# Kernel tuning notes

Hardware: AMD Instinct MI355X
Metric: run time of the kernel (lower is better)

## Reference

```python
import jax, jax.numpy as jnp
import numpy as np

B, N, D, E, HEADS = 2, 256, 768, 8192, 8
HD = D // HEADS
EPS = 1e-5


def _lin(x, w, b):
    return x @ w.T + b


def setup_inputs() -> dict:
    key = jax.random.key(0)
    ks = iter(jax.random.split(key, 64))

    def W(*s):
        return jax.random.normal(next(ks), s, jnp.float32) * 0.02

    inp = {
        "node_embeddings": jax.random.normal(next(ks), (B, N, D), jnp.float32),
        "edge_weights": jax.random.uniform(next(ks), (E,), jnp.float32),
        "edge_indices": jax.random.randint(next(ks), (E, 2), 0, N, jnp.int32),
        # object classifier: D->D->D//2->8
        "oc_w1": W(D, D), "oc_b1": jnp.zeros((D,), jnp.float32),
        "oc_w2": W(D // 2, D), "oc_b2": jnp.zeros((D // 2,), jnp.float32),
        "oc_w3": W(8, D // 2), "oc_b3": jnp.zeros((8,), jnp.float32),
        # importance predictor: D->D//2->D//4->1
        "ip_w1": W(D // 2, D), "ip_b1": jnp.zeros((D // 2,), jnp.float32),
        "ip_w2": W(D // 4, D // 2), "ip_b2": jnp.zeros((D // 4,), jnp.float32),
        "ip_w3": W(1, D // 4), "ip_b3": jnp.zeros((1,), jnp.float32),
        # relation classifier: 2D->D->D//2->8
        "rc_w1": W(D, 2 * D), "rc_b1": jnp.zeros((D,), jnp.float32),
        "rc_w2": W(D // 2, D), "rc_b2": jnp.zeros((D // 2,), jnp.float32),
        "rc_w3": W(8, D // 2), "rc_b3": jnp.zeros((8,), jnp.float32),
        # attention in/out projections
        "attn_in_w": W(3 * D, D), "attn_in_b": jnp.zeros((3 * D,), jnp.float32),
        "attn_out_w": W(D, D), "attn_out_b": jnp.zeros((D,), jnp.float32),
    }
    for l in range(3):
        inp[f"gnn{l}_ws"] = W(D, D)
        inp[f"gnn{l}_bs"] = jnp.zeros((D,), jnp.float32)
        inp[f"gnn{l}_wn"] = W(D, D)
        inp[f"gnn{l}_bn"] = jnp.zeros((D,), jnp.float32)
        inp[f"gnn{l}_g"] = jnp.ones((D,), jnp.float32)
        inp[f"gnn{l}_beta"] = jnp.zeros((D,), jnp.float32)
    return inp


def reference(node_embeddings, edge_weights, edge_indices,
              oc_w1, oc_b1, oc_w2, oc_b2, oc_w3, oc_b3,
              ip_w1, ip_b1, ip_w2, ip_b2, ip_w3, ip_b3,
              rc_w1, rc_b1, rc_w2, rc_b2, rc_w3, rc_b3,
              attn_in_w, attn_in_b, attn_out_w, attn_out_b,
              gnn0_ws, gnn0_bs, gnn0_wn, gnn0_bn, gnn0_g, gnn0_beta,
              gnn1_ws, gnn1_bs, gnn1_wn, gnn1_bn, gnn1_g, gnn1_beta,
              gnn2_ws, gnn2_bs, gnn2_wn, gnn2_bn, gnn2_g, gnn2_beta):
    x = node_embeddings  # [B,N,D]
    src, tgt = edge_indices[:, 0], edge_indices[:, 1]

    # object classifier (dropout is identity in eval)
    h = jax.nn.relu(_lin(x, oc_w1, oc_b1))
    h = jax.nn.relu(_lin(h, oc_w2, oc_b2))
    object_cls = jax.nn.softmax(_lin(h, oc_w3, oc_b3), axis=-1)

    # importance predictor
    h = jax.nn.relu(_lin(x, ip_w1, ip_b1))
    h = jax.nn.relu(_lin(h, ip_w2, ip_b2))
    importance = jax.nn.sigmoid(_lin(h, ip_w3, ip_b3))

    # 3 GNN layers: self-linear + weighted scatter-add neighbor aggregation
    g = x
    layers = [(gnn0_ws, gnn0_bs, gnn0_wn, gnn0_bn, gnn0_g, gnn0_beta),
              (gnn1_ws, gnn1_bs, gnn1_wn, gnn1_bn, gnn1_g, gnn1_beta),
              (gnn2_ws, gnn2_bs, gnn2_wn, gnn2_bn, gnn2_g, gnn2_beta)]
    for ws, bs, wn, bn, gm, bt in layers:
        self_f = _lin(g, ws, bs)
        # vectorized scatter-add: agg[b,tgt] += w_e * g[b,src]
        agg = jnp.zeros_like(g).at[:, tgt, :].add(edge_weights[None, :, None] * g[:, src, :])
        neigh_f = _lin(agg, wn, bn)
        o = jax.nn.relu(self_f + neigh_f)
        mu = o.mean(axis=-1, keepdims=True)
        var = o.var(axis=-1, keepdims=True)  # biased, as torch LayerNorm
        g = gm * (o - mu) / jnp.sqrt(var + EPS) + bt

    # multi-head self-attention (torch MultiheadAttention, batch_first)
    qkv = _lin(g, attn_in_w, attn_in_b)  # [B,N,3D]
    q, k, v = jnp.split(qkv, 3, axis=-1)

    def heads(t):
        return t.reshape(B, N, HEADS, HD).transpose(0, 2, 1, 3)  # [B,H,N,hd]

    q, k, v = heads(q), heads(k), heads(v)
    scores = jnp.einsum('bhqd,bhkd->bhqk', q, k) / jnp.sqrt(jnp.float32(HD))
    attn = jax.nn.softmax(scores, axis=-1)
    ctx = jnp.einsum('bhqk,bhkd->bhqd', attn, v).transpose(0, 2, 1, 3).reshape(B, N, D)
    attended = _lin(ctx, attn_out_w, attn_out_b)  # [B,N,D]
    attn_weights = attn.mean(axis=1)  # torch averages heads -> [B,N,N]

    # all O(N^2) upper-triangular pairs, same (i<j) row-major order as the loop
    ii, jj = np.triu_indices(N, k=1)
    pair = jnp.concatenate([attended[:, ii, :], attended[:, jj, :]], axis=-1)  # [B,P,2D]
    h = jax.nn.relu(_lin(pair, rc_w1, rc_b1))
    h = jax.nn.relu(_lin(h, rc_w2, rc_b2))
    relation = jax.nn.softmax(_lin(h, rc_w3, rc_b3), axis=-1)  # [B,P,8]

    return (object_cls, relation, importance, attended, attn_weights)
```

## Files before the change

kernel.cpp:

```cpp
#include <hip/hip_runtime.h>
#include <hip/hip_bf16.h>

typedef __bf16 bf16;
typedef __bf16 bf16x4 __attribute__((ext_vector_type(4)));
typedef __bf16 bf16x8 __attribute__((ext_vector_type(8)));
typedef float  f32x4  __attribute__((ext_vector_type(4)));

#define NB 2
#define NN 256
#define DD 768
#define EE 8192
#define NPAIR 32640

__device__ inline float wred_sum(float v) {
#pragma unroll
  for (int o = 32; o > 0; o >>= 1) v += __shfl_down(v, o, 64);
  return v;
}
__device__ inline float wred_max(float v) {
#pragma unroll
  for (int o = 32; o > 0; o >>= 1) v = fmaxf(v, __shfl_down(v, o, 64));
  return v;
}

typedef const __attribute__((address_space(1))) void GASV;
typedef __attribute__((address_space(3))) void LASV;
__device__ __forceinline__ void async_cp16(const void* g, void* l) {
  __builtin_amdgcn_global_load_lds((GASV*)g, (LASV*)l, 16, 0, 0);
}

struct CJob { const float* s; bf16* d; int n; };
struct CJobs { CJob j[15]; };
__global__ __launch_bounds__(256) void convert_jobs(CJobs jobs) {
  const CJob jb = jobs.j[blockIdx.y];
  int nv = jb.n >> 2;
  for (int i = blockIdx.x * 256 + threadIdx.x; i < nv; i += gridDim.x * 256) {
    float4 v = ((const float4*)jb.s)[i];
    bf16x4 pk = { (bf16)v.x, (bf16)v.y, (bf16)v.z, (bf16)v.w };
    *(bf16x4*)(jb.d + 4 * i) = pk;
  }
}

__global__ __launch_bounds__(128) void linear_mfma(
    const bf16* __restrict__ X, const bf16* __restrict__ W, int ldw, int wofs,
    const float* __restrict__ bias, const float* __restrict__ addF,
    bf16* __restrict__ outB, float* __restrict__ outF,
    int N, int K, int act)
{
  int tid = threadIdx.x;
  int wave = tid >> 6, lane = tid & 63, lr = lane & 15, lq = lane >> 4;
  int m0 = (blockIdx.x * 2 + wave) * 16;
  int n0 = blockIdx.y * 32;
  const bf16* xrow = X + (size_t)(m0 + lr) * K;
  const bf16* wbase = W + (size_t)wofs;
  f32x4 acc[2] = {};
  for (int k = 0; k < K; k += 32) {
    bf16x8 a = *(const bf16x8*)(xrow + k + lq * 8);
    bf16x8 b0 = *(const bf16x8*)(wbase + (size_t)(n0 + lr) * ldw + k + lq * 8);
    bf16x8 b1 = *(const bf16x8*)(wbase + (size_t)(n0 + 16 + lr) * ldw + k + lq * 8);
    acc[0] = __builtin_amdgcn_mfma_f32_16x16x32_bf16(a, b0, acc[0], 0, 0, 0);
    acc[1] = __builtin_amdgcn_mfma_f32_16x16x32_bf16(a, b1, acc[1], 0, 0, 0);
  }
#pragma unroll
  for (int t = 0; t < 2; ++t) {
    int col = n0 + t * 16 + lr;
    float bv = bias ? bias[col] : 0.0f;
#pragma unroll
    for (int r = 0; r < 4; ++r) {
      int row = m0 + lq * 4 + r;
      size_t o = (size_t)row * N + col;
      float v = acc[t][r] + bv;
      if (addF) v += addF[o];
      if (act) v = fmaxf(v, 0.0f);
      if (outB) outB[o] = (bf16)v;
      if (outF) outF[o] = v;
    }
  }
}

__global__ __launch_bounds__(256) void build_buckets(
    const int* __restrict__ eidx, int* __restrict__ estart, int* __restrict__ bucket)
{
  __shared__ int tg[EE];
  __shared__ int cnt[256];
  __shared__ int sst[257];
  int t = threadIdx.x;
  cnt[t] = 0;
  for (int e = t; e < EE; e += 256) tg[e] = eidx[2 * e + 1];
  __syncthreads();
  for (int e = t; e < EE; e += 256) atomicAdd(&cnt[tg[e]], 1);
  __syncthreads();
  if (t == 0) { int s = 0; for (int i = 0; i < 256; ++i) { sst[i] = s; s += cnt[i]; } sst[256] = s; }
  __syncthreads();
  estart[t] = sst[t];
  if (t == 0) estart[256] = sst[256];
  cnt[t] = sst[t];
  __syncthreads();
  for (int e = t; e < EE; e += 256) {
    int p = atomicAdd(&cnt[tg[e]], 1);
    bucket[p] = e;
  }
}

__global__ __launch_bounds__(256) void gnn_agg(
    const bf16* __restrict__ g, const float* __restrict__ ew, const int* __restrict__ eidx,
    const int* __restrict__ estart, const int* __restrict__ bucket, bf16* __restrict__ agg)
{
  __shared__ int   ssrc[256];
  __shared__ float sw[256];
  int tgt = blockIdx.x, b = blockIdx.y, t = threadIdx.x;
  int s = estart[tgt], e = estart[tgt + 1];
  s = max(0, min(s, EE));
  e = max(s, min(e, EE));
  const bf16* gb = g + (size_t)b * NN * DD;
  float a0 = 0, a1 = 0, a2 = 0, a3 = 0;
  for (int base = s; base < e; base += 256) {
    int nchunk = min(256, e - base);
    if (t < nchunk) {
      int eid = bucket[base + t];
      eid = max(0, min(eid, EE - 1));
      ssrc[t] = eidx[2 * eid] & (NN - 1);
      sw[t] = ew[eid];
    }
    __syncthreads();
    if (t < 192) {
      for (int q = 0; q < nchunk; ++q) {
        float w = sw[q];
        bf16x4 v = *(const bf16x4*)(gb + (size_t)ssrc[q] * DD + 4 * t);
        a0 += w * (float)v[0]; a1 += w * (float)v[1];
        a2 += w * (float)v[2]; a3 += w * (float)v[3];
      }
    }
    __syncthreads();
  }
  if (t < 192) {
    bf16x4 o = { (bf16)a0, (bf16)a1, (bf16)a2, (bf16)a3 };
    *(bf16x4*)(agg + ((size_t)b * NN + tgt) * DD + 4 * t) = o;
  }
}

__global__ __launch_bounds__(256) void layer_norm(
    const float* __restrict__ o, const float* __restrict__ gm,
    const float* __restrict__ bt, bf16* __restrict__ gout)
{
  __shared__ float red[8];
  int row = blockIdx.x, t = threadIdx.x;
  const float* orow = o + (size_t)row * DD;
  float v0 = orow[t], v1 = orow[t + 256], v2 = orow[t + 512];
  float s = v0 + v1 + v2;
  float q = v0 * v0 + v1 * v1 + v2 * v2;
  float ws_ = wred_sum(s), wq = wred_sum(q);
  if ((t & 63) == 0) { red[t >> 6] = ws_; red[4 + (t >> 6)] = wq; }
  __syncthreads();
  float S = red[0] + red[1] + red[2] + red[3];
  float Q = red[4] + red[5] + red[6] + red[7];
  float mu = S * (1.0f / 768.0f);
  float var = Q * (1.0f / 768.0f) - mu * mu;
  float rstd = rsqrtf(var + 1e-5f);
  bf16* gr = gout + (size_t)row * DD;
  gr[t]       = (bf16)(gm[t]       * (v0 - mu) * rstd + bt[t]);
  gr[t + 256] = (bf16)(gm[t + 256] * (v1 - mu) * rstd + bt[t + 256]);
  gr[t + 512] = (bf16)(gm[t + 512] * (v2 - mu) * rstd + bt[t + 512]);
}

__global__ __launch_bounds__(256) void attn_kernel(
    const bf16* __restrict__ qkv, float* __restrict__ probs, bf16* __restrict__ ctx)
{
  __shared__ float qs[96];
  __shared__ float ps[256];
  __shared__ float part[192];
  __shared__ float red[8];
  int qi = blockIdx.x, h = blockIdx.y, b = blockIdx.z, t = threadIdx.x;
  const bf16* qrow = qkv + ((size_t)(b * NN + qi)) * 2304 + h * 96;
  if (t < 96) qs[t] = (float)qrow[t];
  __syncthreads();
  const bf16* krow = qkv + ((size_t)(b * NN + t)) * 2304 + 768 + h * 96;
  float s = 0;
#pragma unroll
  for (int i = 0; i < 12; ++i) {
    bf16x8 kv = *(const bf16x8*)(krow + 8 * i);
#pragma unroll
    for (int j = 0; j < 8; ++j) s += qs[8 * i + j] * (float)kv[j];
  }
  s *= 0.10206207261596577f;
  float wm = wred_max(s);
  if ((t & 63) == 0) red[t >> 6] = wm;
  __syncthreads();
  float MX = fmaxf(fmaxf(red[0], red[1]), fmaxf(red[2], red[3]));
  float e = expf(s - MX);
  float wsum = wred_sum(e);
  if ((t & 63) == 0) red[4 + (t >> 6)] = wsum;
  __syncthreads();
  float SUM = red[4] + red[5] + red[6] + red[7];
  float p = e / SUM;
  ps[t] = p;
  probs[(((size_t)(b * 8 + h) * NN + qi) * NN) + t] = p;
  __syncthreads();
  if (t < 192) {
    int d = t % 96, half = t / 96;
    const bf16* vbase = qkv + (size_t)b * NN * 2304 + 1536 + h * 96 + d;
    float a0 = 0, a1 = 0, a2 = 0, a3 = 0;
    int k0 = half * 128;
    for (int k = k0; k < k0 + 128; k += 4) {
      a0 += ps[k]     * (float)vbase[(size_t)k * 2304];
      a1 += ps[k + 1] * (float)vbase[(size_t)(k + 1) * 2304];
      a2 += ps[k + 2] * (float)vbase[(size_t)(k + 2) * 2304];
      a3 += ps[k + 3] * (float)vbase[(size_t)(k + 3) * 2304];
    }
    part[t] = (a0 + a1) + (a2 + a3);
  }
  __syncthreads();
  if (t < 96)
    ctx[((size_t)(b * NN + qi)) * DD + h * 96 + t] = (bf16)(part[t] + part[t + 96]);
}

__global__ __launch_bounds__(256) void mean_heads(
    const float* __restrict__ probs, float* __restrict__ out)
{
  size_t idx = (size_t)blockIdx.x * 256 + threadIdx.x;
  int k = (int)(idx & 255);
  int qq = (int)((idx >> 8) & 255);
  int b = (int)(idx >> 16);
  float s = 0;
#pragma unroll
  for (int h = 0; h < 8; ++h) s += probs[(((size_t)(b * 8 + h) * NN + qq) * NN) + k];
  out[idx] = s * 0.125f;
}

__global__ __launch_bounds__(256) void fc8_softmax(
    const bf16* __restrict__ h, const float* __restrict__ w,
    const float* __restrict__ bias, float* __restrict__ out)
{
  __shared__ float sw3[8 * 384];
  int t = threadIdx.x;
  for (int i = t; i < 8 * 384; i += 256) sw3[i] = w[i];
  __syncthreads();
  int wave = t >> 6, lane = t & 63;
  int k0 = lane * 6;
#pragma unroll
  for (int i = 0; i < 4; ++i) {
    int r = blockIdx.x * 16 + wave * 4 + i;
    const bf16* hr = h + (size_t)r * 384;
    float hv[6];
#pragma unroll
    for (int j = 0; j < 6; ++j) hv[j] = (float)hr[k0 + j];
    float lg[8];
#pragma unroll
    for (int c = 0; c < 8; ++c) {
      float p = 0;
#pragma unroll
      for (int j = 0; j < 6; ++j) p += hv[j] * sw3[c * 384 + k0 + j];
      lg[c] = wred_sum(p);
    }
    if (lane == 0) {
      float mx = lg[0] + bias[0];
#pragma unroll
      for (int c = 0; c < 8; ++c) { lg[c] += bias[c]; mx = fmaxf(mx, lg[c]); }
      float ex[8], sum = 0;
#pragma unroll
      for (int c = 0; c < 8; ++c) { ex[c] = expf(lg[c] - mx); sum += ex[c]; }
      float inv = 1.0f / sum;
#pragma unroll
      for (int c = 0; c < 8; ++c) out[(size_t)r * 8 + c] = ex[c] * inv;
    }
  }
}

__global__ __launch_bounds__(256) void fc1_sigmoid(
    const bf16* __restrict__ h, const float* __restrict__ w,
    const float* __restrict__ bias, float* __restrict__ out)
{
  __shared__ float sw1[192];
  int t = threadIdx.x;
  if (t < 192) sw1[t] = w[t];
  __syncthreads();
  int wave = t >> 6, lane = t & 63;
  int k0 = lane * 3;
#pragma unroll
  for (int i = 0; i < 4; ++i) {
    int r = blockIdx.x * 16 + wave * 4 + i;
    const bf16* hr = h + (size_t)r * 192;
    float p = (float)hr[k0] * sw1[k0] + (float)hr[k0 + 1] * sw1[k0 + 1]
            + (float)hr[k0 + 2] * sw1[k0 + 2];
    float s = wred_sum(p);
    if (lane == 0) out[r] = 1.0f / (1.0f + expf(-(s + bias[0])));
  }
}

__global__ void make_pairs(int2* __restrict__ pairs)
{
  int i = blockIdx.x;
  int off = i * 255 - (i * (i - 1)) / 2;
  for (int j = i + 1 + threadIdx.x; j < NN; j += blockDim.x)
    pairs[off + (j - i - 1)] = make_int2(i, j);
}

__global__ __launch_bounds__(256) void h2_gemm(
    const bf16* __restrict__ Af, const bf16* __restrict__ Bf,
    const bf16* __restrict__ w2, const float* __restrict__ b2,
    const int2* __restrict__ pairs, bf16* __restrict__ h2)
{
  __shared__ bf16 sh1[128][32];
  __shared__ bf16 sw2[192][32];
  __shared__ int rA[128], rB[128];
  int tid = threadIdx.x;
  int r0 = blockIdx.x * 128;
  int bb = (r0 >= NPAIR) ? 1 : 0;
  int n0 = blockIdx.y * 192;
  if (tid < 128) {
    int2 ij = pairs[r0 - bb * NPAIR + tid];
    rA[tid] = (bb * NN + ij.x) * DD;
    rB[tid] = (bb * NN + ij.y) * DD;
  }
  __syncthreads();
  int row = tid >> 1, kh = (tid & 1) * 16;
  const bf16* ar = Af + rA[row] + kh;
  const bf16* br = Bf + rB[row] + kh;
  char* h1w = (char*)sh1 + row * 64 + (tid & 1) * 32;
  int wave = tid >> 6, lane = tid & 63, lr = lane & 15, lq = lane >> 4;
  int wr = wave >> 1, wc = wave & 1;
  f32x4 acc[4][6] = {};
  for (int k0 = 0; k0 < 768; k0 += 32) {
#pragma unroll
    for (int q = 0; q < 3; ++q)
      async_cp16(w2 + (size_t)(n0 + q * 64 + (tid >> 2)) * 768 + k0 + (tid & 3) * 8,
                 (char*)sw2 + q * 4096 + tid * 16);
    bf16x8 a0 = *(const bf16x8*)(ar + k0);
    bf16x8 a1 = *(const bf16x8*)(ar + k0 + 8);
    bf16x8 b0 = *(const bf16x8*)(br + k0);
    bf16x8 b1 = *(const bf16x8*)(br + k0 + 8);
    bf16x8 h0, h1v;
#pragma unroll
    for (int j = 0; j < 8; ++j) {
      h0[j]  = (bf16)fmaxf((float)a0[j] + (float)b0[j], 0.f);
      h1v[j] = (bf16)fmaxf((float)a1[j] + (float)b1[j], 0.f);
    }
    *(bf16x8*)h1w = h0;
    *(bf16x8*)(h1w + 16) = h1v;
    __syncthreads();
    bf16x8 af[4], bf_[6];
#pragma unroll
    for (int rf = 0; rf < 4; ++rf)
      af[rf] = *(const bf16x8*)((char*)sh1 + (wr * 64 + rf * 16 + lr) * 64 + lq * 16);
#pragma unroll
    for (int cf = 0; cf < 6; ++cf)
      bf_[cf] = *(const bf16x8*)((char*)sw2 + (wc * 96 + cf * 16 + lr) * 64 + lq * 16);
#pragma unroll
    for (int rf = 0; rf < 4; ++rf)
#pragma unroll
      for (int cf = 0; cf < 6; ++cf)
        acc[rf][cf] = __builtin_amdgcn_mfma_f32_16x16x32_bf16(af[rf], bf_[cf], acc[rf][cf], 0, 0, 0);
    __syncthreads();
  }
#pragma unroll
  for (int cf = 0; cf < 6; ++cf) {
    int col = n0 + wc * 96 + cf * 16 + lr;
    float bv = b2[col];
#pragma unroll
    for (int rf = 0; rf < 4; ++rf) {
#pragma unroll
      for (int r = 0; r < 4; ++r) {
        int prow = r0 + wr * 64 + rf * 16 + lq * 4 + r;
        h2[(size_t)prow * 384 + col] = (bf16)fmaxf(acc[rf][cf][r] + bv, 0.f);
      }
    }
  }
}

extern "C" void kernel_launch(void* const* d_in, const int* in_sizes, int n_in,
                              void* d_out, int out_size, void* d_ws, size_t ws_size,
                              hipStream_t stream)
{
  (void)in_sizes; (void)n_in; (void)out_size; (void)ws_size;
  const float* x    = (const float*)d_in[0];
  const float* ew   = (const float*)d_in[1];
  const int*   eidx = (const int*)d_in[2];
  const float* oc_w1 = (const float*)d_in[3];  const float* oc_b1 = (const float*)d_in[4];
  const float* oc_w2 = (const float*)d_in[5];  const float* oc_b2 = (const float*)d_in[6];
  const float* oc_w3 = (const float*)d_in[7];  const float* oc_b3 = (const float*)d_in[8];
  const float* ip_w1 = (const float*)d_in[9];  const float* ip_b1 = (const float*)d_in[10];
  const float* ip_w2 = (const float*)d_in[11]; const float* ip_b2 = (const float*)d_in[12];
  const float* ip_w3 = (const float*)d_in[13]; const float* ip_b3 = (const float*)d_in[14];
  const float* rc_w1 = (const float*)d_in[15]; const float* rc_b1 = (const float*)d_in[16];
  const float* rc_w2 = (const float*)d_in[17]; const float* rc_b2 = (const float*)d_in[18];
  const float* rc_w3 = (const float*)d_in[19]; const float* rc_b3 = (const float*)d_in[20];
  const float* at_iw = (const float*)d_in[21]; const float* at_ib = (const float*)d_in[22];
  const float* at_ow = (const float*)d_in[23]; const float* at_ob = (const float*)d_in[24];

  float* out = (float*)d_out;
  float* out_oc  = out;
  float* out_rel = out + 4096;
  float* out_imp = out + 526336;
  float* out_att = out + 526848;
  float* out_aw  = out + 920064;

  char* wp = (char*)d_ws;
  auto alloc = [&](size_t bytes) { char* p = wp; wp += (bytes + 255) & ~(size_t)255; return p; };
  bf16* h2B  = (bf16*)alloc((size_t)(2 * NPAIR) * 384 * 2);
  float* selfF = (float*)alloc((size_t)512 * 768 * 4);
  float* oBuf  = (float*)alloc((size_t)512 * 768 * 4);
  float* probs = (float*)alloc((size_t)2 * 8 * 256 * 256 * 4);
  bf16* AfB  = (bf16*)alloc((size_t)512 * 768 * 2);
  bf16* BfB  = (bf16*)alloc((size_t)512 * 768 * 2);
  bf16* xb   = (bf16*)alloc((size_t)512 * 768 * 2);
  bf16* g0   = (bf16*)alloc((size_t)512 * 768 * 2);
  bf16* g1   = (bf16*)alloc((size_t)512 * 768 * 2);
  bf16* hA   = (bf16*)alloc((size_t)512 * 768 * 2);
  bf16* hB   = (bf16*)alloc((size_t)512 * 384 * 2);
  bf16* hI1  = (bf16*)alloc((size_t)512 * 384 * 2);
  bf16* hI2  = (bf16*)alloc((size_t)512 * 192 * 2);
  bf16* aggB = (bf16*)alloc((size_t)512 * 768 * 2);
  bf16* qkv  = (bf16*)alloc((size_t)512 * 2304 * 2);
  bf16* ctx  = (bf16*)alloc((size_t)512 * 768 * 2);
  bf16* attB = (bf16*)alloc((size_t)512 * 768 * 2);
  bf16* w_oc1 = (bf16*)alloc((size_t)768 * 768 * 2);
  bf16* w_oc2 = (bf16*)alloc((size_t)384 * 768 * 2);
  bf16* w_ip1 = (bf16*)alloc((size_t)384 * 768 * 2);
  bf16* w_ip2 = (bf16*)alloc((size_t)192 * 384 * 2);
  bf16* w_rc1 = (bf16*)alloc((size_t)768 * 1536 * 2);
  bf16* w_rc2 = (bf16*)alloc((size_t)384 * 768 * 2);
  bf16* w_aiw = (bf16*)alloc((size_t)2304 * 768 * 2);
  bf16* w_aow = (bf16*)alloc((size_t)768 * 768 * 2);
  bf16* w_gnn[6];
  for (int i = 0; i < 6; ++i) w_gnn[i] = (bf16*)alloc((size_t)768 * 768 * 2);
  int2* pairs = (int2*)alloc((size_t)NPAIR * 8);
  int* estart = (int*)alloc(257 * 4);
  int* bucket = (int*)alloc((size_t)EE * 4);

  dim3 blk(256);
  dim3 blk128(128);

  CJobs cj;
  cj.j[0]  = { x,     xb,    512 * 768 };
  cj.j[1]  = { oc_w1, w_oc1, 768 * 768 };
  cj.j[2]  = { oc_w2, w_oc2, 384 * 768 };
  cj.j[3]  = { ip_w1, w_ip1, 384 * 768 };
  cj.j[4]  = { ip_w2, w_ip2, 192 * 384 };
  cj.j[5]  = { rc_w1, w_rc1, 768 * 1536 };
  cj.j[6]  = { rc_w2, w_rc2, 384 * 768 };
  cj.j[7]  = { at_iw, w_aiw, 2304 * 768 };
  cj.j[8]  = { at_ow, w_aow, 768 * 768 };
  for (int l = 0; l < 3; ++l) {
    cj.j[9 + 2 * l]  = { (const float*)d_in[25 + l * 6 + 0], w_gnn[2 * l],     768 * 768 };
    cj.j[10 + 2 * l] = { (const float*)d_in[25 + l * 6 + 2], w_gnn[2 * l + 1], 768 * 768 };
  }
  convert_jobs<<<dim3(128, 15), blk, 0, stream>>>(cj);

  build_buckets<<<1, blk, 0, stream>>>(eidx, estart, bucket);
  make_pairs<<<255, blk, 0, stream>>>(pairs);

  linear_mfma<<<dim3(16, 24), blk128, 0, stream>>>(xb, w_oc1, 768, 0, oc_b1, nullptr, hA, nullptr, 768, 768, 1);
  linear_mfma<<<dim3(16, 12), blk128, 0, stream>>>(hA, w_oc2, 768, 0, oc_b2, nullptr, hB, nullptr, 384, 768, 1);
  fc8_softmax<<<32, blk, 0, stream>>>(hB, oc_w3, oc_b3, out_oc);

  linear_mfma<<<dim3(16, 12), blk128, 0, stream>>>(xb, w_ip1, 768, 0, ip_b1, nullptr, hI1, nullptr, 384, 768, 1);
  linear_mfma<<<dim3(16, 6),  blk128, 0, stream>>>(hI1, w_ip2, 384, 0, ip_b2, nullptr, hI2, nullptr, 192, 384, 1);
  fc1_sigmoid<<<32, blk, 0, stream>>>(hI2, ip_w3, ip_b3, out_imp);

  const bf16* gcur = xb;
  bf16* gbufs[2] = { g0, g1 };
  for (int l = 0; l < 3; ++l) {
    const float* bs_ = (const float*)d_in[25 + l * 6 + 1];
    const float* bn_ = (const float*)d_in[25 + l * 6 + 3];
    const float* gm_ = (const float*)d_in[25 + l * 6 + 4];
    const float* bt_ = (const float*)d_in[25 + l * 6 + 5];
    linear_mfma<<<dim3(16, 24), blk128, 0, stream>>>(gcur, w_gnn[2 * l], 768, 0, bs_, nullptr, nullptr, selfF, 768, 768, 0);
    gnn_agg<<<dim3(256, 2), blk, 0, stream>>>(gcur, ew, eidx, estart, bucket, aggB);
    linear_mfma<<<dim3(16, 24), blk128, 0, stream>>>(aggB, w_gnn[2 * l + 1], 768, 0, bn_, selfF, nullptr, oBuf, 768, 768, 1);
    layer_norm<<<512, blk, 0, stream>>>(oBuf, gm_, bt_, gbufs[l & 1]);
    gcur = gbufs[l & 1];
  }

  linear_mfma<<<dim3(16, 72), blk128, 0, stream>>>(gcur, w_aiw, 768, 0, at_ib, nullptr, qkv, nullptr, 2304, 768, 0);
  attn_kernel<<<dim3(256, 8, 2), blk, 0, stream>>>(qkv, probs, ctx);
  mean_heads<<<512, blk, 0, stream>>>(probs, out_aw);
  linear_mfma<<<dim3(16, 24), blk128, 0, stream>>>(ctx, w_aow, 768, 0, at_ob, nullptr, attB, out_att, 768, 768, 0);

  linear_mfma<<<dim3(16, 24), blk128, 0, stream>>>(attB, w_rc1, 1536, 0,   rc_b1,  nullptr, AfB, nullptr, 768, 768, 0);
  linear_mfma<<<dim3(16, 24), blk128, 0, stream>>>(attB, w_rc1, 1536, 768, nullptr, nullptr, BfB, nullptr, 768, 768, 0);
  h2_gemm<<<dim3(510, 2), blk, 0, stream>>>(AfB, BfB, w_rc2, rc_b2, pairs, h2B);
  fc8_softmax<<<4080, blk, 0, stream>>>(h2B, rc_w3, rc_b3, out_rel);
}
```

Measured before the change: 549.8 us.

## Batch paired linears, fuse head-mean into attention, widen pair GEMM tile

Independent linear layers are now launched together through a two-job kernel that picks its job from blockIdx.z, cutting kernel launches. The per-head probability buffer and the mean_heads kernel are removed: attention atomically accumulates p/8 into the averaged output, which is zeroed with a memset first. The pair GEMM now computes all 384 output columns per 512-thread block, so the relu(A+B) hidden rows are built once instead of twice, and it uses a plane-split LDS layout. The trade-offs are atomic contention and a non-deterministic summation order for the attention weights, plus higher register and LDS pressure per block.

After: 562.3 us. 1.02x slower.

```diff
diff --git a/kernel.cpp b/kernel.cpp
--- a/kernel.cpp
+++ b/kernel.cpp
@@ -41,7 +41,7 @@
   }
 }
 
-__global__ __launch_bounds__(128) void linear_mfma(
+__device__ __forceinline__ void lin_body(
     const bf16* __restrict__ X, const bf16* __restrict__ W, int ldw, int wofs,
     const float* __restrict__ bias, const float* __restrict__ addF,
     bf16* __restrict__ outB, float* __restrict__ outF,
@@ -76,6 +76,27 @@
       if (outF) outF[o] = v;
     }
   }
+}
+
+__global__ __launch_bounds__(128) void linear_mfma(
+    const bf16* __restrict__ X, const bf16* __restrict__ W, int ldw, int wofs,
+    const float* __restrict__ bias, const float* __restrict__ addF,
+    bf16* __restrict__ outB, float* __restrict__ outF,
+    int N, int K, int act)
+{
+  lin_body(X, W, ldw, wofs, bias, addF, outB, outF, N, K, act);
+}
+
+struct LinJob {
+  const bf16* X; const bf16* W; int ldw; int wofs;
+  const float* bias; const float* addF; bf16* outB; float* outF;
+  int N, K, act, gy;
+};
+__global__ __launch_bounds__(128) void linear_mfma2(LinJob j0, LinJob j1)
+{
+  LinJob j = blockIdx.z ? j1 : j0;
+  if ((int)blockIdx.y >= j.gy) return;
+  lin_body(j.X, j.W, j.ldw, j.wofs, j.bias, j.addF, j.outB, j.outF, j.N, j.K, j.act);
 }
 
 __global__ __launch_bounds__(256) void build_buckets(
@@ -164,7 +185,7 @@
 }
 
 __global__ __launch_bounds__(256) void attn_kernel(
-    const bf16* __restrict__ qkv, float* __restrict__ probs, bf16* __restrict__ ctx)
+    const bf16* __restrict__ qkv, float* __restrict__ aw, bf16* __restrict__ ctx)
 {
   __shared__ float qs[96];
   __shared__ float ps[256];
@@ -194,7 +215,7 @@
   float SUM = red[4] + red[5] + red[6] + red[7];
   float p = e / SUM;
   ps[t] = p;
-  probs[(((size_t)(b * 8 + h) * NN + qi) * NN) + t] = p;
+  atomicAdd(&aw[((size_t)(b * NN + qi)) * NN + t], p * 0.125f);
   __syncthreads();
   if (t < 192) {
     int d = t % 96, half = t / 96;
@@ -214,19 +235,6 @@
     ctx[((size_t)(b * NN + qi)) * DD + h * 96 + t] = (bf16)(part[t] + part[t + 96]);
 }
 
-__global__ __launch_bounds__(256) void mean_heads(
-    const float* __restrict__ probs, float* __restrict__ out)
-{
-  size_t idx = (size_t)blockIdx.x * 256 + threadIdx.x;
-  int k = (int)(idx & 255);
-  int qq = (int)((idx >> 8) & 255);
-  int b = (int)(idx >> 16);
-  float s = 0;
-#pragma unroll
-  for (int h = 0; h < 8; ++h) s += probs[(((size_t)(b * 8 + h) * NN + qq) * NN) + k];
-  out[idx] = s * 0.125f;
-}
-
 __global__ __launch_bounds__(256) void fc8_softmax(
     const bf16* __restrict__ h, const float* __restrict__ w,
     const float* __restrict__ bias, float* __restrict__ out)
@@ -295,75 +303,71 @@
     pairs[off + (j - i - 1)] = make_int2(i, j);
 }
 
-__global__ __launch_bounds__(256) void h2_gemm(
+__global__ __launch_bounds__(512) void h2_gemm(
     const bf16* __restrict__ Af, const bf16* __restrict__ Bf,
     const bf16* __restrict__ w2, const float* __restrict__ b2,
     const int2* __restrict__ pairs, bf16* __restrict__ h2)
 {
-  __shared__ bf16 sh1[128][32];
-  __shared__ bf16 sw2[192][32];
+  __shared__ bf16 sh1[4][128][8];
+  __shared__ bf16 sw2[4][384][8];
   __shared__ int rA[128], rB[128];
   int tid = threadIdx.x;
   int r0 = blockIdx.x * 128;
   int bb = (r0 >= NPAIR) ? 1 : 0;
-  int n0 = blockIdx.y * 192;
   if (tid < 128) {
     int2 ij = pairs[r0 - bb * NPAIR + tid];
     rA[tid] = (bb * NN + ij.x) * DD;
     rB[tid] = (bb * NN + ij.y) * DD;
   }
   __syncthreads();
-  int row = tid >> 1, kh = (tid & 1) * 16;
-  const bf16* ar = Af + rA[row] + kh;
-  const bf16* br = Bf + rB[row] + kh;
-  char* h1w = (char*)sh1 + row * 64 + (tid & 1) * 32;
+  int hrow = tid >> 2, hch = tid & 3;
+  const bf16* ar = Af + rA[hrow] + hch * 8;
+  const bf16* br = Bf + rB[hrow] + hch * 8;
+  bf16* h1dst = &sh1[hch][hrow][0];
   int wave = tid >> 6, lane = tid & 63, lr = lane & 15, lq = lane >> 4;
-  int wr = wave >> 1, wc = wave & 1;
+  int wr = wave >> 2, wc = wave & 3;
   f32x4 acc[4][6] = {};
   for (int k0 = 0; k0 < 768; k0 += 32) {
 #pragma unroll
-    for (int q = 0; q < 3; ++q)
-      async_cp16(w2 + (size_t)(n0 + q * 64 + (tid >> 2)) * 768 + k0 + (tid & 3) * 8,
-                 (char*)sw2 + q * 4096 + tid * 16);
-    bf16x8 a0 = *(const bf16x8*)(ar + k0);
-    bf16x8 a1 = *(const bf16x8*)(ar + k0 + 8);
-    bf16x8 b0 = *(const bf16x8*)(br + k0);
-    bf16x8 b1 = *(const bf16x8*)(br + k0 + 8);
-    bf16x8 h0, h1v;
-#pragma unroll
-    for (int j = 0; j < 8; ++j) {
-      h0[j]  = (bf16)fmaxf((float)a0[j] + (float)b0[j], 0.f);
-      h1v[j] = (bf16)fmaxf((float)a1[j] + (float)b1[j], 0.f);
-    }
-    *(bf16x8*)h1w = h0;
-    *(bf16x8*)(h1w + 16) = h1v;
+    for (int q = 0; q < 3; ++q) {
+      int a = q * 512 + tid;
+      int plane = a / 384;
+      int rw = a - plane * 384;
+      async_cp16(w2 + (size_t)rw * 768 + k0 + plane * 8, (char*)sw2 + a * 16);
+    }
+    bf16x8 av = *(const bf16x8*)(ar + k0);
+    bf16x8 bv = *(const bf16x8*)(br + k0);
+    bf16x8 hv;
+#pragma unroll
+    for (int j = 0; j < 8; ++j)
+      hv[j] = (bf16)fmaxf((float)av[j] + (float)bv[j], 0.f);
+    *(bf16x8*)h1dst = hv;
     __syncthreads();
-    bf16x8 af[4], bf_[6];
+    bf16x8 af[4], bfr[6];
 #pragma unroll
     for (int rf = 0; rf < 4; ++rf)
-      af[rf] = *(const bf16x8*)((char*)sh1 + (wr * 64 + rf * 16 + lr) * 64 + lq * 16);
+      af[rf] = *(const bf16x8*)&sh1[lq][wr * 64 + rf * 16 + lr][0];
 #pragma unroll
     for (int cf = 0; cf < 6; ++cf)
-      bf_[cf] = *(const bf16x8*)((char*)sw2 + (wc * 96 + cf * 16 + lr) * 64 + lq * 16);
+      bfr[cf] = *(const bf16x8*)&sw2[lq][wc * 96 + cf * 16 + lr][0];
 #pragma unroll
     for (int rf = 0; rf < 4; ++rf)
 #pragma unroll
       for (int cf = 0; cf < 6; ++cf)
-        acc[rf][cf] = __builtin_amdgcn_mfma_f32_16x16x32_bf16(af[rf], bf_[cf], acc[rf][cf], 0, 0, 0);
+        acc[rf][cf] = __builtin_amdgcn_mfma_f32_16x16x32_bf16(af[rf], bfr[cf], acc[rf][cf], 0, 0, 0);
     __syncthreads();
   }
 #pragma unroll
   for (int cf = 0; cf < 6; ++cf) {
-    int col = n0 + wc * 96 + cf * 16 + lr;
-    float bv = b2[col];
-#pragma unroll
-    for (int rf = 0; rf < 4; ++rf) {
+    int col = wc * 96 + cf * 16 + lr;
+    float bv2 = b2[col];
+#pragma unroll
+    for (int rf = 0; rf < 4; ++rf)
 #pragma unroll
       for (int r = 0; r < 4; ++r) {
         int prow = r0 + wr * 64 + rf * 16 + lq * 4 + r;
-        h2[(size_t)prow * 384 + col] = (bf16)fmaxf(acc[rf][cf][r] + bv, 0.f);
+        h2[(size_t)prow * 384 + col] = (bf16)fmaxf(acc[rf][cf][r] + bv2, 0.f);
       }
-    }
   }
 }
 
@@ -399,7 +403,6 @@
   bf16* h2B  = (bf16*)alloc((size_t)(2 * NPAIR) * 384 * 2);
   float* selfF = (float*)alloc((size_t)512 * 768 * 4);
   float* oBuf  = (float*)alloc((size_t)512 * 768 * 4);
-  float* probs = (float*)alloc((size_t)2 * 8 * 256 * 256 * 4);
   bf16* AfB  = (bf16*)alloc((size_t)512 * 768 * 2);
   bf16* BfB  = (bf16*)alloc((size_t)512 * 768 * 2);
   bf16* xb   = (bf16*)alloc((size_t)512 * 768 * 2);
@@ -445,16 +448,22 @@
     cj.j[10 + 2 * l] = { (const float*)d_in[25 + l * 6 + 2], w_gnn[2 * l + 1], 768 * 768 };
   }
   convert_jobs<<<dim3(128, 15), blk, 0, stream>>>(cj);
+  hipMemsetAsync(out_aw, 0, (size_t)NB * NN * NN * 4, stream);
 
   build_buckets<<<1, blk, 0, stream>>>(eidx, estart, bucket);
   make_pairs<<<255, blk, 0, stream>>>(pairs);
 
-  linear_mfma<<<dim3(16, 24), blk128, 0, stream>>>(xb, w_oc1, 768, 0, oc_b1, nullptr, hA, nullptr, 768, 768, 1);
-  linear_mfma<<<dim3(16, 12), blk128, 0, stream>>>(hA, w_oc2, 768, 0, oc_b2, nullptr, hB, nullptr, 384, 768, 1);
+  {
+    LinJob a = { xb, w_oc1, 768, 0, oc_b1, nullptr, hA,  nullptr, 768, 768, 1, 24 };
+    LinJob b = { xb, w_ip1, 768, 0, ip_b1, nullptr, hI1, nullptr, 384, 768, 1, 12 };
+    linear_mfma2<<<dim3(16, 24, 2), blk128, 0, stream>>>(a, b);
+  }
+  {
+    LinJob a = { hA,  w_oc2, 768, 0, oc_b2, nullptr, hB,  nullptr, 384, 768, 1, 12 };
+    LinJob b = { hI1, w_ip2, 384, 0, ip_b2, nullptr, hI2, nullptr, 192, 384, 1, 6 };
+    linear_mfma2<<<dim3(16, 12, 2), blk128, 0, stream>>>(a, b);
+  }
   fc8_softmax<<<32, blk, 0, stream>>>(hB, oc_w3, oc_b3, out_oc);
-
-  linear_mfma<<<dim3(16, 12), blk128, 0, stream>>>(xb, w_ip1, 768, 0, ip_b1, nullptr, hI1, nullptr, 384, 768, 1);
-  linear_mfma<<<dim3(16, 6),  blk128, 0, stream>>>(hI1, w_ip2, 384, 0, ip_b2, nullptr, hI2, nullptr, 192, 384, 1);
   fc1_sigmoid<<<32, blk, 0, stream>>>(hI2, ip_w3, ip_b3, out_imp);
 
   const bf16* gcur = xb;
@@ -472,12 +481,14 @@
   }
 
   linear_mfma<<<dim3(16, 72), blk128, 0, stream>>>(gcur, w_aiw, 768, 0, at_ib, nullptr, qkv, nullptr, 2304, 768, 0);
-  attn_kernel<<<dim3(256, 8, 2), blk, 0, stream>>>(qkv, probs, ctx);
-  mean_heads<<<512, blk, 0, stream>>>(probs, out_aw);
+  attn_kernel<<<dim3(256, 8, 2), blk, 0, stream>>>(qkv, out_aw, ctx);
   linear_mfma<<<dim3(16, 24), blk128, 0, stream>>>(ctx, w_aow, 768, 0, at_ob, nullptr, attB, out_att, 768, 768, 0);
 
-  linear_mfma<<<dim3(16, 24), blk128, 0, stream>>>(attB, w_rc1, 1536, 0,   rc_b1,  nullptr, AfB, nullptr, 768, 768, 0);
-  linear_mfma<<<dim3(16, 24), blk128, 0, stream>>>(attB, w_rc1, 1536, 768, nullptr, nullptr, BfB, nullptr, 768, 768, 0);
-  h2_gemm<<<dim3(510, 2), blk, 0, stream>>>(AfB, BfB, w_rc2, rc_b2, pairs, h2B);
+  {
+    LinJob a = { attB, w_rc1, 1536, 0,   rc_b1,  nullptr, AfB, nullptr, 768, 768, 0, 24 };
+    LinJob b = { attB, w_rc1, 1536, 768, nullptr, nullptr, BfB, nullptr, 768, 768, 0, 24 };
+    linear_mfma2<<<dim3(16, 24, 2), blk128, 0, stream>>>(a, b);
+  }
+  h2_gemm<<<dim3(510), dim3(512), 0, stream>>>(AfB, BfB, w_rc2, rc_b2, pairs, h2B);
   fc8_softmax<<<4080, blk, 0, stream>>>(h2B, rc_w3, rc_b3, out_rel);
 }
```
